# Performance work log

Measured on AMD Instinct MI355X. Metric: run time of the kernel, lower is better.

## Reference

```python
import jax, jax.numpy as jnp
import numpy as np

B, R, T, D = 256, 36, 64, 1024
EPS_L2 = 1e-8   # lavse l2norm eps
EPS_BN = 1e-5   # torch BatchNorm1d default
LEAK = 0.1      # LeakyReLU slope in ClippedL2Norm


def l2norm(x, axis):
    n = jnp.sqrt(jnp.sum(x * x, axis=axis, keepdims=True)) + EPS_L2
    return x / n


def setup_inputs() -> dict:
    key = jax.random.key(0)
    k1, k2, k3, k4, k5, k6, k7 = jax.random.split(key, 7)
    img_embed = jax.random.normal(k1, (B, R, D), dtype=jnp.float32)
    cap_embed = jax.random.normal(k2, (B, T, D), dtype=jnp.float32)
    lens = jax.random.randint(k3, (B,), 1, T + 1, dtype=jnp.int32)  # at least 1 word
    # nn.Linear(D, 2D): weight (2D, D), bias (2D,)
    lim = 1.0 / np.sqrt(D)
    fc_w = jax.random.uniform(k4, (2 * D, D), jnp.float32, -lim, lim)
    fc_b = jax.random.uniform(k5, (2 * D,), jnp.float32, -lim, lim)
    # BatchNorm1d(D) affine params
    bn_w = jnp.ones((D,), jnp.float32)
    bn_b = jnp.zeros((D,), jnp.float32)
    return {"img_embed": img_embed, "cap_embed": cap_embed, "lens": lens,
            "fc_w": fc_w, "fc_b": fc_b, "bn_w": bn_w, "bn_b": bn_b}


def reference(img_embed, cap_embed, lens, fc_w, fc_b, bn_w, bn_b):
    # permute to channel-first: (B, D, T) / (B, D, R)
    cap = jnp.transpose(cap_embed, (0, 2, 1))
    img = jnp.transpose(img_embed, (0, 2, 1))
    # ClippedL2Norm: leaky relu then l2-normalize along last (token/region) axis
    cap = l2norm(jax.nn.leaky_relu(cap, LEAK), axis=2)
    img = l2norm(jax.nn.leaky_relu(img, LEAK), axis=2)

    t = cap.shape[2]
    mask = (jnp.arange(t)[None, :] < lens[:, None]).astype(cap.dtype)  # (B, T)
    # ragged mean pooling over valid words: (B, D)
    cap_mean = jnp.einsum('bdt,bt->bd', cap, mask) / lens[:, None].astype(cap.dtype)

    # fc(cap).view(D, 2): interleaved alphas/betas
    params = (cap_mean @ fc_w.T + fc_b).reshape(-1, cap.shape[1], 2)  # (B, D, 2)
    alphas, betas = params[..., 0], params[..., 1]                    # (B, D) each

    # BatchNorm1d over (B, D, R) in training mode (batch stats, biased var) — hoisted
    mu = jnp.mean(img, axis=(0, 2))
    var = jnp.mean((img - mu[None, :, None]) ** 2, axis=(0, 2))
    bn = (img - mu[None, :, None]) * (bn_w / jnp.sqrt(var + EPS_BN))[None, :, None] \
         + bn_b[None, :, None]
    base = bn.mean(-1)  # (B_img, D); mean commutes with per-channel affine

    # caption-conditioned affine modulation: (B_cap, B_img, D)
    img_vec = base[None, :, :] * alphas[:, None, :] + betas[:, None, :]
    img_vec = l2norm(img_vec, axis=-1)
    cap_vec = l2norm(cap_mean, axis=-1)  # (B_cap, D)

    # sims[img_j, cap_i] = <img_vec[i, j], cap_vec[i]>
    sims = jnp.einsum('cbd,cd->bc', img_vec, cap_vec)
    return sims
```

## Files before the change

kernel.cpp:

```cpp
#include <hip/hip_runtime.h>
#include <hip/hip_bf16.h>

#define B_ 256
#define R_ 36
#define T_ 64
#define D_ 1024

#define SWZ64(k, c) ((c) ^ ((((k) >> 4) & 3) << 4))
#define SWZ32(k, b) ((b) ^ ((((k) >> 3) & 3) << 3))

__device__ __forceinline__ float lrelu(float x) { return x >= 0.0f ? x : 0.1f * x; }

__device__ __forceinline__ float block_sum(float v, float* sred) {
#pragma unroll
  for (int off = 32; off > 0; off >>= 1) v += __shfl_down(v, off, 64);
  int w = threadIdx.x >> 6;
  if ((threadIdx.x & 63) == 0) sred[w] = v;
  __syncthreads();
  float r = sred[0] + sred[1] + sred[2] + sred[3];
  __syncthreads();
  return r;
}

__global__ __launch_bounds__(256) void input_kernel(const float* __restrict__ cap,
    const float* __restrict__ img, const int* __restrict__ lens,
    float* __restrict__ cap_mean, float* __restrict__ rowsum, float* __restrict__ rowss) {
  __shared__ float4 redA[128], redB[128];
  int bid = blockIdx.x, t = threadIdx.x;
  int rp = t >> 7, dq = t & 127;
  if (bid < 512) {
    int b = bid >> 1, half = bid & 1;
    int len = lens[b];
    const float4* src = reinterpret_cast<const float4*>(cap) +
                        (size_t)b * (T_ * D_ / 4) + half * 128 + dq;
    float4 s2 = {0, 0, 0, 0}, sm = {0, 0, 0, 0};
#pragma unroll 4
    for (int it = 0; it < 32; ++it) {
      int tt = it * 2 + rp;
      float4 v = src[(size_t)tt * 256];
      float y0 = lrelu(v.x), y1 = lrelu(v.y), y2 = lrelu(v.z), y3 = lrelu(v.w);
      s2.x += y0 * y0; s2.y += y1 * y1; s2.z += y2 * y2; s2.w += y3 * y3;
      bool in = tt < len;
      sm.x += in ? y0 : 0.0f; sm.y += in ? y1 : 0.0f;
      sm.z += in ? y2 : 0.0f; sm.w += in ? y3 : 0.0f;
    }
    if (rp) { redA[dq] = s2; redB[dq] = sm; }
    __syncthreads();
    if (!rp) {
      float4 o2 = redA[dq], om = redB[dq];
      s2.x += o2.x; s2.y += o2.y; s2.z += o2.z; s2.w += o2.w;
      sm.x += om.x; sm.y += om.y; sm.z += om.z; sm.w += om.w;
      float il = 1.0f / (float)len;
      float4 cm;
      cm.x = sm.x / (sqrtf(s2.x) + 1e-8f) * il;
      cm.y = sm.y / (sqrtf(s2.y) + 1e-8f) * il;
      cm.z = sm.z / (sqrtf(s2.z) + 1e-8f) * il;
      cm.w = sm.w / (sqrtf(s2.w) + 1e-8f) * il;
      reinterpret_cast<float4*>(cap_mean)[(size_t)b * 256 + half * 128 + dq] = cm;
    }
  } else {
    int bb = bid - 512;
    int b = bb >> 1, half = bb & 1;
    const float4* src = reinterpret_cast<const float4*>(img) +
                        (size_t)b * (R_ * D_ / 4) + half * 128 + dq;
    float4 s1 = {0, 0, 0, 0}, s2 = {0, 0, 0, 0};
#pragma unroll 4
    for (int it = 0; it < 18; ++it) {
      int r = it * 2 + rp;
      float4 v = src[(size_t)r * 256];
      float y0 = lrelu(v.x), y1 = lrelu(v.y), y2 = lrelu(v.z), y3 = lrelu(v.w);
      s1.x += y0; s1.y += y1; s1.z += y2; s1.w += y3;
      s2.x += y0 * y0; s2.y += y1 * y1; s2.z += y2 * y2; s2.w += y3 * y3;
    }
    if (rp) { redA[dq] = s1; redB[dq] = s2; }
    __syncthreads();
    if (!rp) {
      float4 o1 = redA[dq], o2 = redB[dq];
      s1.x += o1.x; s1.y += o1.y; s1.z += o1.z; s1.w += o1.w;
      s2.x += o2.x; s2.y += o2.y; s2.z += o2.z; s2.w += o2.w;
      float n0 = sqrtf(s2.x) + 1e-8f, n1 = sqrtf(s2.y) + 1e-8f;
      float n2 = sqrtf(s2.z) + 1e-8f, n3 = sqrtf(s2.w) + 1e-8f;
      float4 rs, ss;
      rs.x = s1.x / n0; rs.y = s1.y / n1; rs.z = s1.z / n2; rs.w = s1.w / n3;
      ss.x = s2.x / (n0 * n0); ss.y = s2.y / (n1 * n1);
      ss.z = s2.z / (n2 * n2); ss.w = s2.w / (n3 * n3);
      reinterpret_cast<float4*>(rowsum)[(size_t)b * 256 + half * 128 + dq] = rs;
      reinterpret_cast<float4*>(rowss)[(size_t)b * 256 + half * 128 + dq] = ss;
    }
  }
}

__global__ __launch_bounds__(256) void gemm_stats_kernel(
    const float* __restrict__ cap_mean, const float* __restrict__ fc_w,
    const float* __restrict__ rowsum, const float* __restrict__ rowss,
    const float* __restrict__ bn_w, const float* __restrict__ bn_b,
    float* __restrict__ Ppart, float* __restrict__ g, float* __restrict__ h) {
  __shared__ float As[32][64];
  __shared__ float Bs[32][64];
  __shared__ float s1[4][64], s2[4][64];
  int bid = blockIdx.x;
  int t = threadIdx.x;
  if (bid < 512) {
    int nt = bid & 31, ct = (bid >> 5) & 3, kz = bid >> 7;
    int tr = t >> 4, tc = t & 15;
    int cs = t >> 2, k0 = (t & 3) << 3;
    const float* arow = cap_mean + (size_t)(ct * 64 + cs) * D_ + kz * 256;
    const float* brow = fc_w + (size_t)(nt * 64 + cs) * D_ + kz * 256;
    float acc[4][4] = {};
    int sa = SWZ64(k0, cs);
    for (int kb = 0; kb < 256; kb += 32) {
      float4 a0 = *(const float4*)&arow[kb + k0];
      float4 a1 = *(const float4*)&arow[kb + k0 + 4];
      float4 b0 = *(const float4*)&brow[kb + k0];
      float4 b1 = *(const float4*)&brow[kb + k0 + 4];
      __syncthreads();
      As[k0 + 0][sa] = a0.x; As[k0 + 1][sa] = a0.y; As[k0 + 2][sa] = a0.z; As[k0 + 3][sa] = a0.w;
      As[k0 + 4][sa] = a1.x; As[k0 + 5][sa] = a1.y; As[k0 + 6][sa] = a1.z; As[k0 + 7][sa] = a1.w;
      Bs[k0 + 0][sa] = b0.x; Bs[k0 + 1][sa] = b0.y; Bs[k0 + 2][sa] = b0.z; Bs[k0 + 3][sa] = b0.w;
      Bs[k0 + 4][sa] = b1.x; Bs[k0 + 5][sa] = b1.y; Bs[k0 + 6][sa] = b1.z; Bs[k0 + 7][sa] = b1.w;
      __syncthreads();
#pragma unroll
      for (int kk = 0; kk < 32; ++kk) {
        float4 av = *(const float4*)&As[kk][SWZ64(kk, tr * 4)];
        float4 bv = *(const float4*)&Bs[kk][SWZ64(kk, tc * 4)];
        acc[0][0] += av.x * bv.x; acc[0][1] += av.x * bv.y; acc[0][2] += av.x * bv.z; acc[0][3] += av.x * bv.w;
        acc[1][0] += av.y * bv.x; acc[1][1] += av.y * bv.y; acc[1][2] += av.y * bv.z; acc[1][3] += av.y * bv.w;
        acc[2][0] += av.z * bv.x; acc[2][1] += av.z * bv.y; acc[2][2] += av.z * bv.z; acc[2][3] += av.z * bv.w;
        acc[3][0] += av.w * bv.x; acc[3][1] += av.w * bv.y; acc[3][2] += av.w * bv.z; acc[3][3] += av.w * bv.w;
      }
    }
    int c = ct * 64 + tr * 4;
    int n = nt * 64 + tc * 4;
#pragma unroll
    for (int i = 0; i < 4; ++i) {
      *(float4*)&Ppart[((size_t)kz * 256 + c + i) * 2048 + n] =
          make_float4(acc[i][0], acc[i][1], acc[i][2], acc[i][3]);
    }
  } else {
    int sb = bid - 512;
    int dl = t & 63;
    int d = sb * 64 + dl;
    int bg = t >> 6;
    float cs = 0.0f, c2 = 0.0f;
    for (int b = bg * 64; b < bg * 64 + 64; ++b) {
      cs += rowsum[(size_t)b * D_ + d];
      c2 += rowss[(size_t)b * D_ + d];
    }
    s1[bg][dl] = cs;
    s2[bg][dl] = c2;
    __syncthreads();
    if (t < 64) {
      cs = s1[0][dl] + s1[1][dl] + s1[2][dl] + s1[3][dl];
      c2 = s2[0][dl] + s2[1][dl] + s2[2][dl] + s2[3][dl];
      const float inv = 1.0f / (float)(B_ * R_);
      float m = cs * inv, ex2 = c2 * inv;
      float var = ex2 - m * m;
      float gg = bn_w[d] / sqrtf(var + 1e-5f);
      g[d] = gg;
      h[d] = m * gg - bn_b[d];
    }
  }
}

__global__ __launch_bounds__(256) void reduce_scal_kernel(const float* __restrict__ Ppart,
    const float* __restrict__ fc_b, const float* __restrict__ cap_mean,
    float* __restrict__ params, float* __restrict__ rawC, float* __restrict__ BBc,
    float* __restrict__ rn) {
  __shared__ float sred[4], sred2[4], sred3[4];
  int c = blockIdx.x, t = threadIdx.x;
  float4 p0 = reinterpret_cast<const float4*>(fc_b)[2 * t];
  float4 p1 = reinterpret_cast<const float4*>(fc_b)[2 * t + 1];
#pragma unroll
  for (int kz = 0; kz < 4; ++kz) {
    size_t base4 = ((size_t)kz * 256 + c) * 512;
    float4 q0 = reinterpret_cast<const float4*>(Ppart)[base4 + 2 * t];
    float4 q1 = reinterpret_cast<const float4*>(Ppart)[base4 + 2 * t + 1];
    p0.x += q0.x; p0.y += q0.y; p0.z += q0.z; p0.w += q0.w;
    p1.x += q1.x; p1.y += q1.y; p1.z += q1.z; p1.w += q1.w;
  }
  reinterpret_cast<float4*>(params)[(size_t)c * 512 + 2 * t] = p0;
  reinterpret_cast<float4*>(params)[(size_t)c * 512 + 2 * t + 1] = p1;
  float4 cm = reinterpret_cast<const float4*>(cap_mean)[(size_t)c * 256 + t];
  float sBc = p0.y * cm.x + p0.w * cm.y + p1.y * cm.z + p1.w * cm.w;
  float sB2 = p0.y * p0.y + p0.w * p0.w + p1.y * p1.y + p1.w * p1.w;
  float scm = cm.x * cm.x + cm.y * cm.y + cm.z * cm.z + cm.w * cm.w;
  float a = block_sum(sBc, sred);
  float bsum = block_sum(sB2, sred2);
  float cq = block_sum(scm, sred3);
  if (t == 0) {
    rawC[c] = a;
    BBc[c] = bsum;
    rn[c] = 1.0f / (sqrtf(cq) + 1e-8f);
  }
}

__global__ __launch_bounds__(256) void sims_kernel(const float* __restrict__ rowsum,
    const float* __restrict__ g, const float* __restrict__ h,
    const float* __restrict__ params, const float* __restrict__ cap_mean,
    float* __restrict__ Npart, float* __restrict__ Qpart) {
  __shared__ float Tb[64][32];
  __shared__ float Tacv[64][64];
  __shared__ float Ta2[64][64];
  __shared__ float Tab[64][64];
  int t = threadIdx.x;
  int bt = blockIdx.x, ct = blockIdx.y, kz = blockIdx.z;
  int k0 = kz * 64;
  int tr = t >> 4, tc = t & 15;
  int bb = t >> 3, kb = (t & 7) << 3;
  int cc = t >> 2, dc = (t & 3) << 4;
  const float* prow = params + (size_t)(ct * 64 + cc) * 2048 + 2 * k0;
  const float* cmrow = cap_mean + (size_t)(ct * 64 + cc) * 1024 + k0;
  const float* rsrow = rowsum + (size_t)(bt * 32 + bb) * 1024 + k0;
  const float invR = 1.0f / (float)R_;
  {
    float4 v0 = *(const float4*)&rsrow[kb];
    float4 v1 = *(const float4*)&rsrow[kb + 4];
    float4 g0 = *(const float4*)&g[k0 + kb];
    float4 g1 = *(const float4*)&g[k0 + kb + 4];
    float4 h0 = *(const float4*)&h[k0 + kb];
    float4 h1 = *(const float4*)&h[k0 + kb + 4];
    int sb = SWZ32(kb, bb);
    Tb[kb + 0][sb] = v0.x * invR * g0.x - h0.x;
    Tb[kb + 1][sb] = v0.y * invR * g0.y - h0.y;
    Tb[kb + 2][sb] = v0.z * invR * g0.z - h0.z;
    Tb[kb + 3][sb] = v0.w * invR * g0.w - h0.w;
    Tb[kb + 4][sb] = v1.x * invR * g1.x - h1.x;
    Tb[kb + 5][sb] = v1.y * invR * g1.y - h1.y;
    Tb[kb + 6][sb] = v1.z * invR * g1.z - h1.z;
    Tb[kb + 7][sb] = v1.w * invR * g1.w - h1.w;
  }
  int sc = SWZ64(dc, cc);
#pragma unroll
  for (int j = 0; j < 16; j += 4) {
    int d = dc + j;
    float4 p0 = *(const float4*)&prow[2 * d];
    float4 p1 = *(const float4*)&prow[2 * d + 4];
    float4 cm = *(const float4*)&cmrow[d];
    Tacv[d + 0][sc] = p0.x * cm.x; Ta2[d + 0][sc] = p0.x * p0.x; Tab[d + 0][sc] = 2.f * p0.x * p0.y;
    Tacv[d + 1][sc] = p0.z * cm.y; Ta2[d + 1][sc] = p0.z * p0.z; Tab[d + 1][sc] = 2.f * p0.z * p0.w;
    Tacv[d + 2][sc] = p1.x * cm.z; Ta2[d + 2][sc] = p1.x * p1.x; Tab[d + 2][sc] = 2.f * p1.x * p1.y;
    Tacv[d + 3][sc] = p1.z * cm.w; Ta2[d + 3][sc] = p1.z * p1.z; Tab[d + 3][sc] = 2.f * p1.z * p1.w;
  }
  __syncthreads();
  float accN[2][4] = {};
  float accQ[2][4] = {};
#pragma unroll 8
  for (int kk = 0; kk < 64; ++kk) {
    float2 bv = *(const float2*)&Tb[kk][SWZ32(kk, tr * 2)];
    float4 acv = *(const float4*)&Tacv[kk][SWZ64(kk, tc * 4)];
    float4 a2v = *(const float4*)&Ta2[kk][SWZ64(kk, tc * 4)];
    float4 abv = *(const float4*)&Tab[kk][SWZ64(kk, tc * 4)];
    float b0 = bv.x, b1 = bv.y;
    float q0 = b0 * b0, q1 = b1 * b1;
    accN[0][0] += b0 * acv.x; accN[0][1] += b0 * acv.y; accN[0][2] += b0 * acv.z; accN[0][3] += b0 * acv.w;
    accN[1][0] += b1 * acv.x; accN[1][1] += b1 * acv.y; accN[1][2] += b1 * acv.z; accN[1][3] += b1 * acv.w;
    accQ[0][0] += q0 * a2v.x; accQ[0][1] += q0 * a2v.y; accQ[0][2] += q0 * a2v.z; accQ[0][3] += q0 * a2v.w;
    accQ[1][0] += q1 * a2v.x; accQ[1][1] += q1 * a2v.y; accQ[1][2] += q1 * a2v.z; accQ[1][3] += q1 * a2v.w;
    accQ[0][0] += b0 * abv.x; accQ[0][1] += b0 * abv.y; accQ[0][2] += b0 * abv.z; accQ[0][3] += b0 * abv.w;
    accQ[1][0] += b1 * abv.x; accQ[1][1] += b1 * abv.y; accQ[1][2] += b1 * abv.z; accQ[1][3] += b1 * abv.w;
  }
  int br = bt * 32 + tr * 2;
  int c = ct * 64 + tc * 4;
#pragma unroll
  for (int i = 0; i < 2; ++i) {
    size_t o = ((size_t)kz * 256 + br + i) * 256 + c;
    *(float4*)&Npart[o] = make_float4(accN[i][0], accN[i][1], accN[i][2], accN[i][3]);
    *(float4*)&Qpart[o] = make_float4(accQ[i][0], accQ[i][1], accQ[i][2], accQ[i][3]);
  }
}

__global__ __launch_bounds__(256) void final_kernel(const float* __restrict__ Npart,
    const float* __restrict__ Qpart, const float* __restrict__ rawC,
    const float* __restrict__ BBc, const float* __restrict__ rn, float* __restrict__ out) {
  int b = blockIdx.x, c = threadIdx.x;
  float N = rawC[c], Q = BBc[c];
#pragma unroll
  for (int kz = 0; kz < 16; ++kz) {
    size_t o = ((size_t)kz * 256 + b) * 256 + c;
    N += Npart[o];
    Q += Qpart[o];
  }
  out[b * 256 + c] = N * rn[c] / (sqrtf(Q) + 1e-8f);
}

extern "C" void kernel_launch(void* const* d_in, const int* in_sizes, int n_in,
                              void* d_out, int out_size, void* d_ws, size_t ws_size,
                              hipStream_t stream) {
  const float* img = (const float*)d_in[0];
  const float* cap = (const float*)d_in[1];
  const int* lens = (const int*)d_in[2];
  const float* fc_w = (const float*)d_in[3];
  const float* fc_b = (const float*)d_in[4];
  const float* bn_w = (const float*)d_in[5];
  const float* bn_b = (const float*)d_in[6];
  float* out = (float*)d_out;
  float* ws = (float*)d_ws;

  float* cap_mean = ws;
  float* rowsum   = ws + 262144;
  float* rowss    = ws + 524288;
  float* g        = ws + 786432;
  float* h        = ws + 787456;
  float* params   = ws + 788480;
  float* rawC     = ws + 1312768;
  float* BBc      = ws + 1313024;
  float* rn       = ws + 1313280;
  float* region   = ws + 1313536;
  float* Ppart    = region;
  float* Npart    = region;
  float* Qpart    = region + 1048576;

  input_kernel<<<1024, 256, 0, stream>>>(cap, img, lens, cap_mean, rowsum, rowss);
  gemm_stats_kernel<<<528, 256, 0, stream>>>(cap_mean, fc_w, rowsum, rowss,
                                             bn_w, bn_b, Ppart, g, h);
  reduce_scal_kernel<<<256, 256, 0, stream>>>(Ppart, fc_b, cap_mean, params,
                                              rawC, BBc, rn);
  sims_kernel<<<dim3(8, 4, 16), 256, 0, stream>>>(rowsum, g, h, params, cap_mean,
                                                  Npart, Qpart);
  final_kernel<<<256, 256, 0, stream>>>(Npart, Qpart, rawC, BBc, rn, out);
}
```

Measured before the change: 65.06 us.

## Fuse split-K partial reduction and per-caption scalars into sims and final kernels

New measurement: 77.75 us. 1.2x slower.

```diff
diff --git a/kernel.cpp b/kernel.cpp
--- a/kernel.cpp
+++ b/kernel.cpp
@@ -10,17 +10,6 @@
 #define SWZ32(k, b) ((b) ^ ((((k) >> 3) & 3) << 3))
 
 __device__ __forceinline__ float lrelu(float x) { return x >= 0.0f ? x : 0.1f * x; }
-
-__device__ __forceinline__ float block_sum(float v, float* sred) {
-#pragma unroll
-  for (int off = 32; off > 0; off >>= 1) v += __shfl_down(v, off, 64);
-  int w = threadIdx.x >> 6;
-  if ((threadIdx.x & 63) == 0) sred[w] = v;
-  __syncthreads();
-  float r = sred[0] + sred[1] + sred[2] + sred[3];
-  __syncthreads();
-  return r;
-}
 
 __global__ __launch_bounds__(256) void input_kernel(const float* __restrict__ cap,
     const float* __restrict__ img, const int* __restrict__ lens,
@@ -162,42 +151,11 @@
   }
 }
 
-__global__ __launch_bounds__(256) void reduce_scal_kernel(const float* __restrict__ Ppart,
-    const float* __restrict__ fc_b, const float* __restrict__ cap_mean,
-    float* __restrict__ params, float* __restrict__ rawC, float* __restrict__ BBc,
-    float* __restrict__ rn) {
-  __shared__ float sred[4], sred2[4], sred3[4];
-  int c = blockIdx.x, t = threadIdx.x;
-  float4 p0 = reinterpret_cast<const float4*>(fc_b)[2 * t];
-  float4 p1 = reinterpret_cast<const float4*>(fc_b)[2 * t + 1];
-#pragma unroll
-  for (int kz = 0; kz < 4; ++kz) {
-    size_t base4 = ((size_t)kz * 256 + c) * 512;
-    float4 q0 = reinterpret_cast<const float4*>(Ppart)[base4 + 2 * t];
-    float4 q1 = reinterpret_cast<const float4*>(Ppart)[base4 + 2 * t + 1];
-    p0.x += q0.x; p0.y += q0.y; p0.z += q0.z; p0.w += q0.w;
-    p1.x += q1.x; p1.y += q1.y; p1.z += q1.z; p1.w += q1.w;
-  }
-  reinterpret_cast<float4*>(params)[(size_t)c * 512 + 2 * t] = p0;
-  reinterpret_cast<float4*>(params)[(size_t)c * 512 + 2 * t + 1] = p1;
-  float4 cm = reinterpret_cast<const float4*>(cap_mean)[(size_t)c * 256 + t];
-  float sBc = p0.y * cm.x + p0.w * cm.y + p1.y * cm.z + p1.w * cm.w;
-  float sB2 = p0.y * p0.y + p0.w * p0.w + p1.y * p1.y + p1.w * p1.w;
-  float scm = cm.x * cm.x + cm.y * cm.y + cm.z * cm.z + cm.w * cm.w;
-  float a = block_sum(sBc, sred);
-  float bsum = block_sum(sB2, sred2);
-  float cq = block_sum(scm, sred3);
-  if (t == 0) {
-    rawC[c] = a;
-    BBc[c] = bsum;
-    rn[c] = 1.0f / (sqrtf(cq) + 1e-8f);
-  }
-}
-
 __global__ __launch_bounds__(256) void sims_kernel(const float* __restrict__ rowsum,
     const float* __restrict__ g, const float* __restrict__ h,
-    const float* __restrict__ params, const float* __restrict__ cap_mean,
-    float* __restrict__ Npart, float* __restrict__ Qpart) {
+    const float* __restrict__ Ppart, const float* __restrict__ fc_b,
+    const float* __restrict__ cap_mean,
+    float* __restrict__ Npart, float* __restrict__ Qpart, float* __restrict__ Spart) {
   __shared__ float Tb[64][32];
   __shared__ float Tacv[64][64];
   __shared__ float Ta2[64][64];
@@ -208,9 +166,9 @@
   int tr = t >> 4, tc = t & 15;
   int bb = t >> 3, kb = (t & 7) << 3;
   int cc = t >> 2, dc = (t & 3) << 4;
-  const float* prow = params + (size_t)(ct * 64 + cc) * 2048 + 2 * k0;
   const float* cmrow = cap_mean + (size_t)(ct * 64 + cc) * 1024 + k0;
   const float* rsrow = rowsum + (size_t)(bt * 32 + bb) * 1024 + k0;
+  size_t prowoff = (size_t)(ct * 64 + cc) * 2048 + 2 * (size_t)k0;
   const float invR = 1.0f / (float)R_;
   {
     float4 v0 = *(const float4*)&rsrow[kb];
@@ -230,16 +188,39 @@
     Tb[kb + 7][sb] = v1.w * invR * g1.w - h1.w;
   }
   int sc = SWZ64(dc, cc);
+  float sBc = 0.0f, sB2 = 0.0f, scm = 0.0f;
 #pragma unroll
   for (int j = 0; j < 16; j += 4) {
     int d = dc + j;
-    float4 p0 = *(const float4*)&prow[2 * d];
-    float4 p1 = *(const float4*)&prow[2 * d + 4];
     float4 cm = *(const float4*)&cmrow[d];
+    float4 p0 = *(const float4*)&fc_b[2 * (k0 + d)];
+    float4 p1 = *(const float4*)&fc_b[2 * (k0 + d) + 4];
+#pragma unroll
+    for (int s4 = 0; s4 < 4; ++s4) {
+      const float* sl = Ppart + (size_t)s4 * 524288 + prowoff + 2 * d;
+      float4 q0 = *(const float4*)sl;
+      float4 q1 = *(const float4*)(sl + 4);
+      p0.x += q0.x; p0.y += q0.y; p0.z += q0.z; p0.w += q0.w;
+      p1.x += q1.x; p1.y += q1.y; p1.z += q1.z; p1.w += q1.w;
+    }
     Tacv[d + 0][sc] = p0.x * cm.x; Ta2[d + 0][sc] = p0.x * p0.x; Tab[d + 0][sc] = 2.f * p0.x * p0.y;
     Tacv[d + 1][sc] = p0.z * cm.y; Ta2[d + 1][sc] = p0.z * p0.z; Tab[d + 1][sc] = 2.f * p0.z * p0.w;
     Tacv[d + 2][sc] = p1.x * cm.z; Ta2[d + 2][sc] = p1.x * p1.x; Tab[d + 2][sc] = 2.f * p1.x * p1.y;
     Tacv[d + 3][sc] = p1.z * cm.w; Ta2[d + 3][sc] = p1.z * p1.z; Tab[d + 3][sc] = 2.f * p1.z * p1.w;
+    sBc += p0.y * cm.x + p0.w * cm.y + p1.y * cm.z + p1.w * cm.w;
+    sB2 += p0.y * p0.y + p0.w * p0.w + p1.y * p1.y + p1.w * p1.w;
+    scm += cm.x * cm.x + cm.y * cm.y + cm.z * cm.z + cm.w * cm.w;
+  }
+  if (bt == 0) {
+    sBc += __shfl_down(sBc, 2, 4); sBc += __shfl_down(sBc, 1, 4);
+    sB2 += __shfl_down(sB2, 2, 4); sB2 += __shfl_down(sB2, 1, 4);
+    scm += __shfl_down(scm, 2, 4); scm += __shfl_down(scm, 1, 4);
+    if ((t & 3) == 0) {
+      size_t so = ((size_t)kz * 256 + ct * 64 + cc) * 4;
+      Spart[so + 0] = sBc;
+      Spart[so + 1] = sB2;
+      Spart[so + 2] = scm;
+    }
   }
   __syncthreads();
   float accN[2][4] = {};
@@ -270,17 +251,26 @@
 }
 
 __global__ __launch_bounds__(256) void final_kernel(const float* __restrict__ Npart,
-    const float* __restrict__ Qpart, const float* __restrict__ rawC,
-    const float* __restrict__ BBc, const float* __restrict__ rn, float* __restrict__ out) {
+    const float* __restrict__ Qpart, const float* __restrict__ Spart,
+    float* __restrict__ out) {
   int b = blockIdx.x, c = threadIdx.x;
-  float N = rawC[c], Q = BBc[c];
+  float sBc = 0.0f, sB2 = 0.0f, scm = 0.0f;
+#pragma unroll
+  for (int kz = 0; kz < 16; ++kz) {
+    size_t so = ((size_t)kz * 256 + c) * 4;
+    sBc += Spart[so + 0];
+    sB2 += Spart[so + 1];
+    scm += Spart[so + 2];
+  }
+  float rn = 1.0f / (sqrtf(scm) + 1e-8f);
+  float N = sBc, Q = sB2;
 #pragma unroll
   for (int kz = 0; kz < 16; ++kz) {
     size_t o = ((size_t)kz * 256 + b) * 256 + c;
     N += Npart[o];
     Q += Qpart[o];
   }
-  out[b * 256 + c] = N * rn[c] / (sqrtf(Q) + 1e-8f);
+  out[b * 256 + c] = N * rn / (sqrtf(Q) + 1e-8f);
 }
 
 extern "C" void kernel_launch(void* const* d_in, const int* in_sizes, int n_in,
@@ -301,21 +291,15 @@
   float* rowss    = ws + 524288;
   float* g        = ws + 786432;
   float* h        = ws + 787456;
-  float* params   = ws + 788480;
-  float* rawC     = ws + 1312768;
-  float* BBc      = ws + 1313024;
-  float* rn       = ws + 1313280;
-  float* region   = ws + 1313536;
-  float* Ppart    = region;
-  float* Npart    = region;
-  float* Qpart    = region + 1048576;
+  float* Spart    = ws + 788480;
+  float* Ppart    = ws + 804864;
+  float* Npart    = ws + 2902016;
+  float* Qpart    = ws + 3950592;
 
   input_kernel<<<1024, 256, 0, stream>>>(cap, img, lens, cap_mean, rowsum, rowss);
   gemm_stats_kernel<<<528, 256, 0, stream>>>(cap_mean, fc_w, rowsum, rowss,
                                              bn_w, bn_b, Ppart, g, h);
-  reduce_scal_kernel<<<256, 256, 0, stream>>>(Ppart, fc_b, cap_mean, params,
-                                              rawC, BBc, rn);
-  sims_kernel<<<dim3(8, 4, 16), 256, 0, stream>>>(rowsum, g, h, params, cap_mean,
-                                                  Npart, Qpart);
-  final_kernel<<<256, 256, 0, stream>>>(Npart, Qpart, rawC, BBc, rn, out);
-}
+  sims_kernel<<<dim3(8, 4, 16), 256, 0, stream>>>(rowsum, g, h, Ppart, fc_b,
+                                                  cap_mean, Npart, Qpart, Spart);
+  final_kernel<<<256, 256, 0, stream>>>(Npart, Qpart, Spart, out);
+}
```

## Enlarge GEMM tile to 128x128 with 8x8 register blocking and deeper split-K

Applied to the files above, without the earlier changes.

Measured after the change: 66.50 us. 2.2% more time.

```diff
diff --git a/kernel.cpp b/kernel.cpp
--- a/kernel.cpp
+++ b/kernel.cpp
@@ -8,6 +8,7 @@
 
 #define SWZ64(k, c) ((c) ^ ((((k) >> 4) & 3) << 4))
 #define SWZ32(k, b) ((b) ^ ((((k) >> 3) & 3) << 3))
+#define SWZG(k, c)  ((c) ^ ((((k) >> 3) & 3) << 2))
 
 __device__ __forceinline__ float lrelu(float x) { return x >= 0.0f ? x : 0.1f * x; }
 
@@ -95,49 +96,68 @@
     const float* __restrict__ rowsum, const float* __restrict__ rowss,
     const float* __restrict__ bn_w, const float* __restrict__ bn_b,
     float* __restrict__ Ppart, float* __restrict__ g, float* __restrict__ h) {
-  __shared__ float As[32][64];
-  __shared__ float Bs[32][64];
-  __shared__ float s1[4][64], s2[4][64];
+  __shared__ float As[32][128];
+  __shared__ float Bs[32][128];
+  __shared__ float s1s[4][64], s2s[4][64];
   int bid = blockIdx.x;
   int t = threadIdx.x;
-  if (bid < 512) {
-    int nt = bid & 31, ct = (bid >> 5) & 3, kz = bid >> 7;
+  if (bid < 256) {
+    int nt = bid & 15, ct = (bid >> 4) & 1, kz = bid >> 5;
     int tr = t >> 4, tc = t & 15;
-    int cs = t >> 2, k0 = (t & 3) << 3;
-    const float* arow = cap_mean + (size_t)(ct * 64 + cs) * D_ + kz * 256;
-    const float* brow = fc_w + (size_t)(nt * 64 + cs) * D_ + kz * 256;
-    float acc[4][4] = {};
-    int sa = SWZ64(k0, cs);
-    for (int kb = 0; kb < 256; kb += 32) {
-      float4 a0 = *(const float4*)&arow[kb + k0];
-      float4 a1 = *(const float4*)&arow[kb + k0 + 4];
-      float4 b0 = *(const float4*)&brow[kb + k0];
-      float4 b1 = *(const float4*)&brow[kb + k0 + 4];
+    int ca = t >> 2, k0 = (t & 3) << 3;
+    const float* arow0 = cap_mean + (size_t)(ct * 128 + ca) * D_ + kz * 128;
+    const float* arow1 = arow0 + (size_t)64 * D_;
+    const float* brow0 = fc_w + (size_t)(nt * 128 + ca) * D_ + kz * 128;
+    const float* brow1 = brow0 + (size_t)64 * D_;
+    float acc[8][8] = {};
+    int sa0 = SWZG(k0, ca);
+    int sa1 = SWZG(k0, ca + 64);
+    for (int kb = 0; kb < 128; kb += 32) {
+      float4 a0 = *(const float4*)&arow0[kb + k0];
+      float4 a1 = *(const float4*)&arow0[kb + k0 + 4];
+      float4 a2 = *(const float4*)&arow1[kb + k0];
+      float4 a3 = *(const float4*)&arow1[kb + k0 + 4];
+      float4 b0 = *(const float4*)&brow0[kb + k0];
+      float4 b1 = *(const float4*)&brow0[kb + k0 + 4];
+      float4 b2 = *(const float4*)&brow1[kb + k0];
+      float4 b3 = *(const float4*)&brow1[kb + k0 + 4];
       __syncthreads();
-      As[k0 + 0][sa] = a0.x; As[k0 + 1][sa] = a0.y; As[k0 + 2][sa] = a0.z; As[k0 + 3][sa] = a0.w;
-      As[k0 + 4][sa] = a1.x; As[k0 + 5][sa] = a1.y; As[k0 + 6][sa] = a1.z; As[k0 + 7][sa] = a1.w;
-      Bs[k0 + 0][sa] = b0.x; Bs[k0 + 1][sa] = b0.y; Bs[k0 + 2][sa] = b0.z; Bs[k0 + 3][sa] = b0.w;
-      Bs[k0 + 4][sa] = b1.x; Bs[k0 + 5][sa] = b1.y; Bs[k0 + 6][sa] = b1.z; Bs[k0 + 7][sa] = b1.w;
+      As[k0 + 0][sa0] = a0.x; As[k0 + 1][sa0] = a0.y; As[k0 + 2][sa0] = a0.z; As[k0 + 3][sa0] = a0.w;
+      As[k0 + 4][sa0] = a1.x; As[k0 + 5][sa0] = a1.y; As[k0 + 6][sa0] = a1.z; As[k0 + 7][sa0] = a1.w;
+      As[k0 + 0][sa1] = a2.x; As[k0 + 1][sa1] = a2.y; As[k0 + 2][sa1] = a2.z; As[k0 + 3][sa1] = a2.w;
+      As[k0 + 4][sa1] = a3.x; As[k0 + 5][sa1] = a3.y; As[k0 + 6][sa1] = a3.z; As[k0 + 7][sa1] = a3.w;
+      Bs[k0 + 0][sa0] = b0.x; Bs[k0 + 1][sa0] = b0.y; Bs[k0 + 2][sa0] = b0.z; Bs[k0 + 3][sa0] = b0.w;
+      Bs[k0 + 4][sa0] = b1.x; Bs[k0 + 5][sa0] = b1.y; Bs[k0 + 6][sa0] = b1.z; Bs[k0 + 7][sa0] = b1.w;
+      Bs[k0 + 0][sa1] = b2.x; Bs[k0 + 1][sa1] = b2.y; Bs[k0 + 2][sa1] = b2.z; Bs[k0 + 3][sa1] = b2.w;
+      Bs[k0 + 4][sa1] = b3.x; Bs[k0 + 5][sa1] = b3.y; Bs[k0 + 6][sa1] = b3.z; Bs[k0 + 7][sa1] = b3.w;
       __syncthreads();
 #pragma unroll
       for (int kk = 0; kk < 32; ++kk) {
-        float4 av = *(const float4*)&As[kk][SWZ64(kk, tr * 4)];
-        float4 bv = *(const float4*)&Bs[kk][SWZ64(kk, tc * 4)];
-        acc[0][0] += av.x * bv.x; acc[0][1] += av.x * bv.y; acc[0][2] += av.x * bv.z; acc[0][3] += av.x * bv.w;
-        acc[1][0] += av.y * bv.x; acc[1][1] += av.y * bv.y; acc[1][2] += av.y * bv.z; acc[1][3] += av.y * bv.w;
-        acc[2][0] += av.z * bv.x; acc[2][1] += av.z * bv.y; acc[2][2] += av.z * bv.z; acc[2][3] += av.z * bv.w;
-        acc[3][0] += av.w * bv.x; acc[3][1] += av.w * bv.y; acc[3][2] += av.w * bv.z; acc[3][3] += av.w * bv.w;
+        int col0 = (tr * 4) ^ (((kk >> 3) & 3) << 2);
+        int col1 = (tc * 4) ^ (((kk >> 3) & 3) << 2);
+        float4 av0 = *(const float4*)&As[kk][col0];
+        float4 av1 = *(const float4*)&As[kk][col0 + 64];
+        float4 bv0 = *(const float4*)&Bs[kk][col1];
+        float4 bv1 = *(const float4*)&Bs[kk][col1 + 64];
+        float ar[8] = {av0.x, av0.y, av0.z, av0.w, av1.x, av1.y, av1.z, av1.w};
+        float br[8] = {bv0.x, bv0.y, bv0.z, bv0.w, bv1.x, bv1.y, bv1.z, bv1.w};
+#pragma unroll
+        for (int i = 0; i < 8; ++i)
+#pragma unroll
+          for (int j = 0; j < 8; ++j) acc[i][j] += ar[i] * br[j];
       }
     }
-    int c = ct * 64 + tr * 4;
-    int n = nt * 64 + tc * 4;
-#pragma unroll
-    for (int i = 0; i < 4; ++i) {
-      *(float4*)&Ppart[((size_t)kz * 256 + c + i) * 2048 + n] =
-          make_float4(acc[i][0], acc[i][1], acc[i][2], acc[i][3]);
+    int cbase = ct * 128 + tr * 4;
+    int nbase = nt * 128 + tc * 4;
+#pragma unroll
+    for (int i = 0; i < 8; ++i) {
+      int c = cbase + (i & 3) + ((i >> 2) << 6);
+      size_t o = ((size_t)kz * 256 + c) * 2048 + nbase;
+      *(float4*)&Ppart[o] = make_float4(acc[i][0], acc[i][1], acc[i][2], acc[i][3]);
+      *(float4*)&Ppart[o + 64] = make_float4(acc[i][4], acc[i][5], acc[i][6], acc[i][7]);
     }
   } else {
-    int sb = bid - 512;
+    int sb = bid - 256;
     int dl = t & 63;
     int d = sb * 64 + dl;
     int bg = t >> 6;
@@ -146,12 +166,12 @@
       cs += rowsum[(size_t)b * D_ + d];
       c2 += rowss[(size_t)b * D_ + d];
     }
-    s1[bg][dl] = cs;
-    s2[bg][dl] = c2;
+    s1s[bg][dl] = cs;
+    s2s[bg][dl] = c2;
     __syncthreads();
     if (t < 64) {
-      cs = s1[0][dl] + s1[1][dl] + s1[2][dl] + s1[3][dl];
-      c2 = s2[0][dl] + s2[1][dl] + s2[2][dl] + s2[3][dl];
+      cs = s1s[0][dl] + s1s[1][dl] + s1s[2][dl] + s1s[3][dl];
+      c2 = s2s[0][dl] + s2s[1][dl] + s2s[2][dl] + s2s[3][dl];
       const float inv = 1.0f / (float)(B_ * R_);
       float m = cs * inv, ex2 = c2 * inv;
       float var = ex2 - m * m;
@@ -171,7 +191,7 @@
   float4 p0 = reinterpret_cast<const float4*>(fc_b)[2 * t];
   float4 p1 = reinterpret_cast<const float4*>(fc_b)[2 * t + 1];
 #pragma unroll
-  for (int kz = 0; kz < 4; ++kz) {
+  for (int kz = 0; kz < 8; ++kz) {
     size_t base4 = ((size_t)kz * 256 + c) * 512;
     float4 q0 = reinterpret_cast<const float4*>(Ppart)[base4 + 2 * t];
     float4 q1 = reinterpret_cast<const float4*>(Ppart)[base4 + 2 * t + 1];
@@ -305,13 +325,12 @@
   float* rawC     = ws + 1312768;
   float* BBc      = ws + 1313024;
   float* rn       = ws + 1313280;
-  float* region   = ws + 1313536;
-  float* Ppart    = region;
-  float* Npart    = region;
-  float* Qpart    = region + 1048576;
+  float* Ppart    = ws + 1313536;
+  float* Npart    = ws + 5507840;
+  float* Qpart    = ws + 6556416;
 
   input_kernel<<<1024, 256, 0, stream>>>(cap, img, lens, cap_mean, rowsum, rowss);
-  gemm_stats_kernel<<<528, 256, 0, stream>>>(cap_mean, fc_w, rowsum, rowss,
+  gemm_stats_kernel<<<272, 256, 0, stream>>>(cap_mean, fc_w, rowsum, rowss,
                                              bn_w, bn_b, Ppart, g, h);
   reduce_scal_kernel<<<256, 256, 0, stream>>>(Ppart, fc_b, cap_mean, params,
                                               rawC, BBc, rn);
```

## Drop split-K GEMM and fold reduction kernel into GEMM and final epilogues

Applied to the files above, without the earlier changes.

After: 70.76 us. 8.8% more time.

```diff
diff --git a/kernel.cpp b/kernel.cpp
--- a/kernel.cpp
+++ b/kernel.cpp
@@ -24,8 +24,10 @@
 
 __global__ __launch_bounds__(256) void input_kernel(const float* __restrict__ cap,
     const float* __restrict__ img, const int* __restrict__ lens,
-    float* __restrict__ cap_mean, float* __restrict__ rowsum, float* __restrict__ rowss) {
+    float* __restrict__ cap_mean, float* __restrict__ rowsum, float* __restrict__ rowss,
+    float* __restrict__ scmp) {
   __shared__ float4 redA[128], redB[128];
+  __shared__ float sred[4];
   int bid = blockIdx.x, t = threadIdx.x;
   int rp = t >> 7, dq = t & 127;
   if (bid < 512) {
@@ -46,6 +48,7 @@
     }
     if (rp) { redA[dq] = s2; redB[dq] = sm; }
     __syncthreads();
+    float sq = 0.0f;
     if (!rp) {
       float4 o2 = redA[dq], om = redB[dq];
       s2.x += o2.x; s2.y += o2.y; s2.z += o2.z; s2.w += o2.w;
@@ -57,7 +60,11 @@
       cm.z = sm.z / (sqrtf(s2.z) + 1e-8f) * il;
       cm.w = sm.w / (sqrtf(s2.w) + 1e-8f) * il;
       reinterpret_cast<float4*>(cap_mean)[(size_t)b * 256 + half * 128 + dq] = cm;
-    }
+      sq = cm.x * cm.x + cm.y * cm.y + cm.z * cm.z + cm.w * cm.w;
+    }
+    __syncthreads();
+    float tot = block_sum(sq, sred);
+    if (t == 0) scmp[bid] = tot;
   } else {
     int bb = bid - 512;
     int b = bb >> 1, half = bb & 1;
@@ -94,64 +101,91 @@
     const float* __restrict__ cap_mean, const float* __restrict__ fc_w,
     const float* __restrict__ rowsum, const float* __restrict__ rowss,
     const float* __restrict__ bn_w, const float* __restrict__ bn_b,
-    float* __restrict__ Ppart, float* __restrict__ g, float* __restrict__ h) {
-  __shared__ float As[32][64];
+    const float* __restrict__ fc_b, float* __restrict__ params,
+    float* __restrict__ Spart, float* __restrict__ g, float* __restrict__ h) {
+  __shared__ float As[32][33];
   __shared__ float Bs[32][64];
-  __shared__ float s1[4][64], s2[4][64];
-  int bid = blockIdx.x;
-  int t = threadIdx.x;
-  if (bid < 512) {
-    int nt = bid & 31, ct = (bid >> 5) & 3, kz = bid >> 7;
+  __shared__ float s1s[4][64], s2s[4][64];
+  int bid = blockIdx.x, t = threadIdx.x;
+  if (bid < 256) {
+    int nt = bid & 31, ct = bid >> 5;
     int tr = t >> 4, tc = t & 15;
-    int cs = t >> 2, k0 = (t & 3) << 3;
-    const float* arow = cap_mean + (size_t)(ct * 64 + cs) * D_ + kz * 256;
-    const float* brow = fc_w + (size_t)(nt * 64 + cs) * D_ + kz * 256;
-    float acc[4][4] = {};
-    int sa = SWZ64(k0, cs);
-    for (int kb = 0; kb < 256; kb += 32) {
-      float4 a0 = *(const float4*)&arow[kb + k0];
-      float4 a1 = *(const float4*)&arow[kb + k0 + 4];
-      float4 b0 = *(const float4*)&brow[kb + k0];
-      float4 b1 = *(const float4*)&brow[kb + k0 + 4];
+    int ar = t >> 3, ak = (t & 7) << 2;
+    int nb = t >> 2, kb0 = (t & 3) << 3;
+    const float* arow = cap_mean + (size_t)(ct * 32 + ar) * D_;
+    const float* brow = fc_w + (size_t)(nt * 64 + nb) * D_;
+    int sb = SWZ64(kb0, nb);
+    float acc[2][4] = {};
+    float4 apf = *(const float4*)&arow[ak];
+    float4 bpf0 = *(const float4*)&brow[kb0];
+    float4 bpf1 = *(const float4*)&brow[kb0 + 4];
+    for (int ch = 0; ch < 32; ++ch) {
       __syncthreads();
-      As[k0 + 0][sa] = a0.x; As[k0 + 1][sa] = a0.y; As[k0 + 2][sa] = a0.z; As[k0 + 3][sa] = a0.w;
-      As[k0 + 4][sa] = a1.x; As[k0 + 5][sa] = a1.y; As[k0 + 6][sa] = a1.z; As[k0 + 7][sa] = a1.w;
-      Bs[k0 + 0][sa] = b0.x; Bs[k0 + 1][sa] = b0.y; Bs[k0 + 2][sa] = b0.z; Bs[k0 + 3][sa] = b0.w;
-      Bs[k0 + 4][sa] = b1.x; Bs[k0 + 5][sa] = b1.y; Bs[k0 + 6][sa] = b1.z; Bs[k0 + 7][sa] = b1.w;
+      As[ak + 0][ar] = apf.x; As[ak + 1][ar] = apf.y;
+      As[ak + 2][ar] = apf.z; As[ak + 3][ar] = apf.w;
+      Bs[kb0 + 0][sb] = bpf0.x; Bs[kb0 + 1][sb] = bpf0.y;
+      Bs[kb0 + 2][sb] = bpf0.z; Bs[kb0 + 3][sb] = bpf0.w;
+      Bs[kb0 + 4][sb] = bpf1.x; Bs[kb0 + 5][sb] = bpf1.y;
+      Bs[kb0 + 6][sb] = bpf1.z; Bs[kb0 + 7][sb] = bpf1.w;
       __syncthreads();
+      if (ch < 31) {
+        int ko = (ch + 1) * 32;
+        apf = *(const float4*)&arow[ko + ak];
+        bpf0 = *(const float4*)&brow[ko + kb0];
+        bpf1 = *(const float4*)&brow[ko + kb0 + 4];
+      }
 #pragma unroll
       for (int kk = 0; kk < 32; ++kk) {
-        float4 av = *(const float4*)&As[kk][SWZ64(kk, tr * 4)];
+        float a0 = As[kk][tr * 2];
+        float a1 = As[kk][tr * 2 + 1];
         float4 bv = *(const float4*)&Bs[kk][SWZ64(kk, tc * 4)];
-        acc[0][0] += av.x * bv.x; acc[0][1] += av.x * bv.y; acc[0][2] += av.x * bv.z; acc[0][3] += av.x * bv.w;
-        acc[1][0] += av.y * bv.x; acc[1][1] += av.y * bv.y; acc[1][2] += av.y * bv.z; acc[1][3] += av.y * bv.w;
-        acc[2][0] += av.z * bv.x; acc[2][1] += av.z * bv.y; acc[2][2] += av.z * bv.z; acc[2][3] += av.z * bv.w;
-        acc[3][0] += av.w * bv.x; acc[3][1] += av.w * bv.y; acc[3][2] += av.w * bv.z; acc[3][3] += av.w * bv.w;
+        acc[0][0] += a0 * bv.x; acc[0][1] += a0 * bv.y; acc[0][2] += a0 * bv.z; acc[0][3] += a0 * bv.w;
+        acc[1][0] += a1 * bv.x; acc[1][1] += a1 * bv.y; acc[1][2] += a1 * bv.z; acc[1][3] += a1 * bv.w;
       }
     }
-    int c = ct * 64 + tr * 4;
     int n = nt * 64 + tc * 4;
-#pragma unroll
-    for (int i = 0; i < 4; ++i) {
-      *(float4*)&Ppart[((size_t)kz * 256 + c + i) * 2048 + n] =
-          make_float4(acc[i][0], acc[i][1], acc[i][2], acc[i][3]);
+    int c0 = ct * 32 + tr * 2;
+    float4 fb = *(const float4*)&fc_b[n];
+    float4 p0 = make_float4(acc[0][0] + fb.x, acc[0][1] + fb.y, acc[0][2] + fb.z, acc[0][3] + fb.w);
+    float4 p1 = make_float4(acc[1][0] + fb.x, acc[1][1] + fb.y, acc[1][2] + fb.z, acc[1][3] + fb.w);
+    *(float4*)&params[(size_t)c0 * 2048 + n] = p0;
+    *(float4*)&params[(size_t)(c0 + 1) * 2048 + n] = p1;
+    int d0 = nt * 32 + tc * 2;
+    float2 cmA = *(const float2*)&cap_mean[(size_t)c0 * 1024 + d0];
+    float2 cmB = *(const float2*)&cap_mean[(size_t)(c0 + 1) * 1024 + d0];
+    float sBc0 = p0.y * cmA.x + p0.w * cmA.y;
+    float sB20 = p0.y * p0.y + p0.w * p0.w;
+    float sBc1 = p1.y * cmB.x + p1.w * cmB.y;
+    float sB21 = p1.y * p1.y + p1.w * p1.w;
+#pragma unroll
+    for (int off = 8; off > 0; off >>= 1) {
+      sBc0 += __shfl_down(sBc0, off, 16);
+      sB20 += __shfl_down(sB20, off, 16);
+      sBc1 += __shfl_down(sBc1, off, 16);
+      sB21 += __shfl_down(sB21, off, 16);
+    }
+    if (tc == 0) {
+      Spart[nt * 256 + c0] = sBc0;
+      Spart[nt * 256 + c0 + 1] = sBc1;
+      Spart[8192 + nt * 256 + c0] = sB20;
+      Spart[8192 + nt * 256 + c0 + 1] = sB21;
     }
   } else {
-    int sb = bid - 512;
+    int sbk = bid - 256;
     int dl = t & 63;
-    int d = sb * 64 + dl;
+    int d = sbk * 64 + dl;
     int bg = t >> 6;
     float cs = 0.0f, c2 = 0.0f;
     for (int b = bg * 64; b < bg * 64 + 64; ++b) {
       cs += rowsum[(size_t)b * D_ + d];
       c2 += rowss[(size_t)b * D_ + d];
     }
-    s1[bg][dl] = cs;
-    s2[bg][dl] = c2;
+    s1s[bg][dl] = cs;
+    s2s[bg][dl] = c2;
     __syncthreads();
     if (t < 64) {
-      cs = s1[0][dl] + s1[1][dl] + s1[2][dl] + s1[3][dl];
-      c2 = s2[0][dl] + s2[1][dl] + s2[2][dl] + s2[3][dl];
+      cs = s1s[0][dl] + s1s[1][dl] + s1s[2][dl] + s1s[3][dl];
+      c2 = s2s[0][dl] + s2s[1][dl] + s2s[2][dl] + s2s[3][dl];
       const float inv = 1.0f / (float)(B_ * R_);
       float m = cs * inv, ex2 = c2 * inv;
       float var = ex2 - m * m;
@@ -159,38 +193,6 @@
       g[d] = gg;
       h[d] = m * gg - bn_b[d];
     }
-  }
-}
-
-__global__ __launch_bounds__(256) void reduce_scal_kernel(const float* __restrict__ Ppart,
-    const float* __restrict__ fc_b, const float* __restrict__ cap_mean,
-    float* __restrict__ params, float* __restrict__ rawC, float* __restrict__ BBc,
-    float* __restrict__ rn) {
-  __shared__ float sred[4], sred2[4], sred3[4];
-  int c = blockIdx.x, t = threadIdx.x;
-  float4 p0 = reinterpret_cast<const float4*>(fc_b)[2 * t];
-  float4 p1 = reinterpret_cast<const float4*>(fc_b)[2 * t + 1];
-#pragma unroll
-  for (int kz = 0; kz < 4; ++kz) {
-    size_t base4 = ((size_t)kz * 256 + c) * 512;
-    float4 q0 = reinterpret_cast<const float4*>(Ppart)[base4 + 2 * t];
-    float4 q1 = reinterpret_cast<const float4*>(Ppart)[base4 + 2 * t + 1];
-    p0.x += q0.x; p0.y += q0.y; p0.z += q0.z; p0.w += q0.w;
-    p1.x += q1.x; p1.y += q1.y; p1.z += q1.z; p1.w += q1.w;
-  }
-  reinterpret_cast<float4*>(params)[(size_t)c * 512 + 2 * t] = p0;
-  reinterpret_cast<float4*>(params)[(size_t)c * 512 + 2 * t + 1] = p1;
-  float4 cm = reinterpret_cast<const float4*>(cap_mean)[(size_t)c * 256 + t];
-  float sBc = p0.y * cm.x + p0.w * cm.y + p1.y * cm.z + p1.w * cm.w;
-  float sB2 = p0.y * p0.y + p0.w * p0.w + p1.y * p1.y + p1.w * p1.w;
-  float scm = cm.x * cm.x + cm.y * cm.y + cm.z * cm.z + cm.w * cm.w;
-  float a = block_sum(sBc, sred);
-  float bsum = block_sum(sB2, sred2);
-  float cq = block_sum(scm, sred3);
-  if (t == 0) {
-    rawC[c] = a;
-    BBc[c] = bsum;
-    rn[c] = 1.0f / (sqrtf(cq) + 1e-8f);
   }
 }
 
@@ -270,17 +272,25 @@
 }
 
 __global__ __launch_bounds__(256) void final_kernel(const float* __restrict__ Npart,
-    const float* __restrict__ Qpart, const float* __restrict__ rawC,
-    const float* __restrict__ BBc, const float* __restrict__ rn, float* __restrict__ out) {
+    const float* __restrict__ Qpart, const float* __restrict__ Spart,
+    const float* __restrict__ scmp, float* __restrict__ out) {
   int b = blockIdx.x, c = threadIdx.x;
-  float N = rawC[c], Q = BBc[c];
+  float sBc = 0.0f, sB2 = 0.0f;
+#pragma unroll
+  for (int nt = 0; nt < 32; ++nt) {
+    sBc += Spart[nt * 256 + c];
+    sB2 += Spart[8192 + nt * 256 + c];
+  }
+  float scm = scmp[2 * c] + scmp[2 * c + 1];
+  float rn = 1.0f / (sqrtf(scm) + 1e-8f);
+  float N = sBc, Q = sB2;
 #pragma unroll
   for (int kz = 0; kz < 16; ++kz) {
     size_t o = ((size_t)kz * 256 + b) * 256 + c;
     N += Npart[o];
     Q += Qpart[o];
   }
-  out[b * 256 + c] = N * rn[c] / (sqrtf(Q) + 1e-8f);
+  out[b * 256 + c] = N * rn / (sqrtf(Q) + 1e-8f);
 }
 
 extern "C" void kernel_launch(void* const* d_in, const int* in_sizes, int n_in,
@@ -301,21 +311,17 @@
   float* rowss    = ws + 524288;
   float* g        = ws + 786432;
   float* h        = ws + 787456;
-  float* params   = ws + 788480;
-  float* rawC     = ws + 1312768;
-  float* BBc      = ws + 1313024;
-  float* rn       = ws + 1313280;
-  float* region   = ws + 1313536;
-  float* Ppart    = region;
-  float* Npart    = region;
-  float* Qpart    = region + 1048576;
-
-  input_kernel<<<1024, 256, 0, stream>>>(cap, img, lens, cap_mean, rowsum, rowss);
-  gemm_stats_kernel<<<528, 256, 0, stream>>>(cap_mean, fc_w, rowsum, rowss,
-                                             bn_w, bn_b, Ppart, g, h);
-  reduce_scal_kernel<<<256, 256, 0, stream>>>(Ppart, fc_b, cap_mean, params,
-                                              rawC, BBc, rn);
+  float* scmp     = ws + 788480;
+  float* Spart    = ws + 788992;
+  float* params   = ws + 805376;
+  float* Npart    = ws + 1329664;
+  float* Qpart    = ws + 2378240;
+
+  input_kernel<<<1024, 256, 0, stream>>>(cap, img, lens, cap_mean, rowsum, rowss,
+                                         scmp);
+  gemm_stats_kernel<<<272, 256, 0, stream>>>(cap_mean, fc_w, rowsum, rowss,
+                                             bn_w, bn_b, fc_b, params, Spart, g, h);
   sims_kernel<<<dim3(8, 4, 16), 256, 0, stream>>>(rowsum, g, h, params, cap_mean,
                                                   Npart, Qpart);
-  final_kernel<<<256, 256, 0, stream>>>(Npart, Qpart, rawC, BBc, rn, out);
-}
+  final_kernel<<<256, 256, 0, stream>>>(Npart, Qpart, Spart, scmp, out);
+}
```
